# Optimization experiments

Measured on AMD Instinct MI355X. Metric: run time of the kernel, lower is better.

The kernel has to match this reference:

```python
import jax, jax.numpy as jnp
import numpy as np

S, DM, H, DH, FF, L = 2048, 1024, 16, 64, 4096, 2
N_IMG, GH, GW = 4, 16, 32  # 4 images, each 16x32=512 tokens
THETA = 10000.0
LN_EPS = 1e-5


def _rope_tables():
    # 2D repeated rope: dim=DH, dim//4 freqs, x/y angles interleaved -> DH//2 per token
    fr = 1.0 / THETA ** (np.arange(0, DH, 4)[: DH // 4] / DH)  # [DH//4]
    pos = np.arange(GH * GW)
    xang = np.outer(pos % GW, fr)   # [512, DH//4]
    yang = np.outer(pos // GW, fr)  # [512, DH//4]
    ang = np.stack([xang, yang], axis=-1).reshape(GH * GW, DH // 2)  # [512, DH//2]
    ang = np.tile(ang, (N_IMG, 1))  # same grid repeated per image -> [S, DH//2]
    return np.cos(ang).astype(np.float32), np.sin(ang).astype(np.float32)


def setup_inputs() -> dict:
    key = jax.random.key(0)
    ks = jax.random.split(key, 8)
    scale = 0.02

    def rn(k, shape):
        return jax.random.normal(k, shape, jnp.float32) * scale

    x = jax.random.normal(ks[0], (S, DM), jnp.float32)
    input_row_offsets = jnp.array([0, 512, 1024, 1536, 2048], jnp.int32)
    cos_np, sin_np = _rope_tables()
    inp = {
        "x": x,
        "input_row_offsets": input_row_offsets,
        "freqs_cos": jnp.asarray(cos_np),
        "freqs_sin": jnp.asarray(sin_np),
        # stacked per-layer params [L, ...]; Linear weights stored as [in, out]
        "ln0_g": jnp.ones((L, DM), jnp.float32),
        "ln0_b": jnp.zeros((L, DM), jnp.float32),
        "ln1_g": jnp.ones((L, DM), jnp.float32),
        "ln1_b": jnp.zeros((L, DM), jnp.float32),
        "wqkv_w": rn(ks[1], (L, DM, 3 * DM)),
        "wqkv_b": jnp.zeros((L, 3 * DM), jnp.float32),
        "wo_w": rn(ks[2], (L, DM, DM)),
        "wo_b": jnp.zeros((L, DM), jnp.float32),
        "up_w": rn(ks[3], (L, DM, FF)),
        "up_b": jnp.zeros((L, FF), jnp.float32),
        "down_w": rn(ks[4], (L, FF, DM)),
        "down_b": jnp.zeros((L, DM), jnp.float32),
        "lnf_g": jnp.ones((DM,), jnp.float32),
        "lnf_b": jnp.zeros((DM,), jnp.float32),
    }
    return inp


def _layernorm(v, g, b):
    m = v.mean(-1, keepdims=True)
    var = v.var(-1, keepdims=True)
    return (v - m) * jax.lax.rsqrt(var + LN_EPS) * g + b


def _rope(t, cos, sin):
    # t: [S, H, DH]; pairs (even, odd) rotated by complex freqs (broadcast over heads)
    tr = t.reshape(S, H, DH // 2, 2)
    te, to = tr[..., 0], tr[..., 1]
    c = cos[:, None, :]
    s = sin[:, None, :]
    oe = te * c - to * s
    oo = te * s + to * c
    return jnp.stack([oe, oo], axis=-1).reshape(S, H, DH)


def reference(x, input_row_offsets, freqs_cos, freqs_sin,
              ln0_g, ln0_b, ln1_g, ln1_b, wqkv_w, wqkv_b, wo_w, wo_b,
              up_w, up_b, down_w, down_b, lnf_g, lnf_b):
    # Block-diagonal mask. NOTE: the torch reference ADDS the boolean mask
    # (True -> +1.0) to the logits, it does NOT mask with -inf. Replicated faithfully.
    seg = jnp.searchsorted(input_row_offsets, jnp.arange(S), side="right")
    maskf = (seg[:, None] == seg[None, :]).astype(jnp.float32)  # [S, S]
    inv_sqrt_d = 1.0 / jnp.sqrt(jnp.float32(DH))

    def layer(h, p):
        g0, b0, g1, b1, Wqkv, bqkv, Wo, bo, Wu, bu, Wd, bd = p
        y = _layernorm(h, g0, b0)
        qkv = (y @ Wqkv + bqkv).reshape(S, 3, H, DH)
        q, k, v = qkv[:, 0], qkv[:, 1], qkv[:, 2]
        q = _rope(q, freqs_cos, freqs_sin)
        k = _rope(k, freqs_cos, freqs_sin)
        aw = jnp.einsum("shd,thd->hst", q, k) * inv_sqrt_d + maskf[None]  # [H,S,S]
        aw = jax.nn.softmax(aw.astype(jnp.float32), axis=-1).astype(q.dtype)
        ao = jnp.einsum("hst,thd->shd", aw, v).reshape(S, DM)
        h = h + ao @ Wo + bo
        y = _layernorm(h, g1, b1)
        y = jax.nn.gelu(y @ Wu + bu, approximate=True)
        h = h + y @ Wd + bd
        return h, None

    params = (ln0_g, ln0_b, ln1_g, ln1_b, wqkv_w, wqkv_b, wo_w, wo_b,
              up_w, up_b, down_w, down_b)
    h, _ = jax.lax.scan(layer, x, params)
    return _layernorm(h, lnf_g, lnf_b)
```

## Files before the change

### kernel.cpp

```cpp
#include <hip/hip_runtime.h>
#include <hip/hip_bf16.h>
#include <stdint.h>
#include <math.h>

#define S_LEN 2048
#define DMODEL 1024
#define NHEAD 16
#define DHEAD 64
#define FFDIM 4096
#define NLAYER 2

using bf16 = __hip_bfloat16;
typedef __attribute__((ext_vector_type(8))) short bf16x8;
typedef __attribute__((ext_vector_type(4))) float f32x4;
typedef __attribute__((ext_vector_type(16))) float f32x16;
typedef __attribute__((ext_vector_type(4))) int i32x4;

#define MFMA16x16(A, B, C) __builtin_amdgcn_mfma_f32_16x16x32_bf16(A, B, C, 0, 0, 0)
#define MFMA32x32(A, B, C) __builtin_amdgcn_mfma_f32_32x32x16_bf16(A, B, C, 0, 0, 0)
#define EXP2(x) __builtin_amdgcn_exp2f(x)

__device__ __forceinline__ float bf2f(uint32_t u16bits) {
  union { uint32_t i; float f; } x;
  x.i = u16bits << 16;
  return x.f;
}
__device__ __forceinline__ uint16_t f2bf(float f) {
  return __builtin_bit_cast(uint16_t, __float2bfloat16(f));
}

__device__ __forceinline__ uint32_t cvtpk(float lo, float hi) {
  uint32_t r;
  asm("v_cvt_pk_bf16_f32 %0, %1, %2" : "=v"(r) : "v"(lo), "v"(hi));
  return r;
}
__device__ __forceinline__ void pl32swap(uint32_t& a, uint32_t& b) {
#if __has_builtin(__builtin_amdgcn_permlane32_swap)
  typedef __attribute__((ext_vector_type(2))) int i32x2;
  i32x2 r = __builtin_amdgcn_permlane32_swap((int)a, (int)b, false, false);
  a = (uint32_t)r.x;
  b = (uint32_t)r.y;
#else
  asm volatile("v_permlane32_swap_b32 %0, %1" : "+v"(a), "+v"(b));
#endif
}

__global__ __launch_bounds__(256) void k_tcast(const float* __restrict__ in,
                                               bf16* __restrict__ out,
                                               int R, int C) {
  __shared__ float tl[32][33];
  int t = threadIdx.x;
  int r0 = blockIdx.y * 32, c0 = blockIdx.x * 32;
  int cl = t & 31, rl = t >> 5;
#pragma unroll
  for (int i = 0; i < 4; ++i)
    tl[rl + i * 8][cl] = in[(size_t)(r0 + rl + i * 8) * C + c0 + cl];
  __syncthreads();
#pragma unroll
  for (int i = 0; i < 4; ++i)
    out[(size_t)(c0 + rl + i * 8) * R + r0 + cl] = __float2bfloat16(tl[cl][rl + i * 8]);
}

__device__ __forceinline__ void ln_store4(bf16* p, float a, float b, float c, float d) {
  uint2 u;
  u.x = (uint32_t)f2bf(a) | ((uint32_t)f2bf(b) << 16);
  u.y = (uint32_t)f2bf(c) | ((uint32_t)f2bf(d) << 16);
  *(uint2*)p = u;
}
__device__ __forceinline__ void ln_store4(float* p, float a, float b, float c, float d) {
  *(float4*)p = make_float4(a, b, c, d);
}

template <typename OUT>
__global__ __launch_bounds__(256) void k_ln(const float* __restrict__ h,
                                            const float* __restrict__ g,
                                            const float* __restrict__ b,
                                            OUT* __restrict__ y) {
  int row = blockIdx.x, t = threadIdx.x;
  const float4 v = ((const float4*)(h + (size_t)row * DMODEL))[t];
  float s = v.x + v.y + v.z + v.w;
  float s2 = v.x * v.x + v.y * v.y + v.z * v.z + v.w * v.w;
#pragma unroll
  for (int off = 32; off > 0; off >>= 1) {
    s += __shfl_down(s, off);
    s2 += __shfl_down(s2, off);
  }
  __shared__ float red[8];
  int w = t >> 6;
  if ((t & 63) == 0) { red[w] = s; red[4 + w] = s2; }
  __syncthreads();
  s = red[0] + red[1] + red[2] + red[3];
  s2 = red[4] + red[5] + red[6] + red[7];
  float mean = s * (1.0f / DMODEL);
  float var = s2 * (1.0f / DMODEL) - mean * mean;
  float rstd = rsqrtf(var + 1e-5f);
  float4 gv = ((const float4*)g)[t];
  float4 bv = ((const float4*)b)[t];
  float o0 = (v.x - mean) * rstd * gv.x + bv.x;
  float o1 = (v.y - mean) * rstd * gv.y + bv.y;
  float o2 = (v.z - mean) * rstd * gv.z + bv.z;
  float o3 = (v.w - mean) * rstd * gv.w + bv.w;
  ln_store4(y + (size_t)row * DMODEL + t * 4, o0, o1, o2, o3);
}

__global__ __launch_bounds__(256) void k_rope(const bf16* __restrict__ qkv,
                                              const float* __restrict__ fcos,
                                              const float* __restrict__ fsin,
                                              bf16* __restrict__ qr,
                                              bf16* __restrict__ kr) {
  int idx = blockIdx.x * 256 + threadIdx.x;
  int p = idx & 31;
  int hh = (idx >> 5) & (NHEAD - 1);
  int s = idx >> 9;
  float c = fcos[s * 32 + p], sn = fsin[s * 32 + p];
  int colq = hh * DHEAD + 2 * p;
  uint32_t rq = *(const uint32_t*)(qkv + (size_t)s * 3 * DMODEL + colq);
  uint32_t rk = *(const uint32_t*)(qkv + (size_t)s * 3 * DMODEL + DMODEL + colq);
  {
    float te = bf2f(rq & 0xffffu), to = bf2f(rq >> 16);
    uint32_t outv = (uint32_t)f2bf(te * c - to * sn) | ((uint32_t)f2bf(te * sn + to * c) << 16);
    *(uint32_t*)(qr + (size_t)s * DMODEL + colq) = outv;
  }
  {
    float te = bf2f(rk & 0xffffu), to = bf2f(rk >> 16);
    uint32_t outv = (uint32_t)f2bf(te * c - to * sn) | ((uint32_t)f2bf(te * sn + to * c) << 16);
    *(uint32_t*)(kr + (size_t)s * DMODEL + colq) = outv;
  }
}

__global__ __launch_bounds__(256) void k_tv(const bf16* __restrict__ qkv,
                                            bf16* __restrict__ vT) {
  __shared__ bf16 tl[64][65];
  int t = threadIdx.x;
  int hh = blockIdx.y;
  int sb = blockIdx.x * 64;
#pragma unroll
  for (int i = 0; i < 16; ++i) {
    int e = i * 256 + t;
    int sl = e >> 6, d = e & 63;
    tl[sl][d] = qkv[(size_t)(sb + sl) * 3 * DMODEL + 2 * DMODEL + hh * DHEAD + d];
  }
  __syncthreads();
#pragma unroll
  for (int i = 0; i < 16; ++i) {
    int e = i * 256 + t;
    int d = e >> 6, sl = e & 63;
    vT[(size_t)(hh * DHEAD + d) * S_LEN + sb + sl] = tl[sl][d];
  }
}

template <int EPI, int BM>
__global__ __launch_bounds__(256) void k_gemm2(const bf16* __restrict__ A,
                                               const bf16* __restrict__ BT,
                                               const float* __restrict__ bias,
                                               void* __restrict__ out,
                                               int M, int N, int K, int Kc) {
  constexpr int MF = BM / 32;
  __shared__ bf16 As[2][BM * 64];
  __shared__ bf16 Bs[2][128 * 64];
  int t = threadIdx.x;
  int w = t >> 6, l = t & 63, lr = l & 15, lg = l >> 4;

  int nxy = gridDim.x * gridDim.y;
  int bid = blockIdx.y * gridDim.x + blockIdx.x;
  int chk8 = nxy >> 3;
  int swz = (bid & 7) * chk8 + (bid >> 3);
  int bx = swz % gridDim.x, by = swz / gridDim.x;
  int bm = bx * BM, bn = by * 128;
  int k0 = blockIdx.z * Kc;
  int wm = (w >> 1) * (BM / 2), wn = (w & 1) * 64;

  f32x4 zero4 = {0.f, 0.f, 0.f, 0.f};
  f32x4 acc[MF][4];
#pragma unroll
  for (int mf = 0; mf < MF; ++mf)
#pragma unroll
    for (int nf = 0; nf < 4; ++nf) acc[mf][nf] = zero4;

  auto stage = [&](int buf, int kk) {
#pragma unroll
    for (int i = 0; i < BM / 32; ++i) {
      int chunk = i * 256 + t;
      int row = chunk >> 3;
      int scol = ((chunk ^ row) & 7) << 3;
      __builtin_amdgcn_global_load_lds(
          (__attribute__((address_space(1))) void*)(A + (size_t)(bm + row) * K + kk + scol),
          (__attribute__((address_space(3))) void*)(&As[buf][chunk * 8]), 16, 0, 0);
    }
#pragma unroll
    for (int i = 0; i < 4; ++i) {
      int chunk = i * 256 + t;
      int row = chunk >> 3;
      int scol = ((chunk ^ row) & 7) << 3;
      __builtin_amdgcn_global_load_lds(
          (__attribute__((address_space(1))) void*)(BT + (size_t)(bn + row) * K + kk + scol),
          (__attribute__((address_space(3))) void*)(&Bs[buf][chunk * 8]), 16, 0, 0);
    }
  };

  int nt = Kc / 64;
  stage(0, k0);
  __syncthreads();
  int cur = 0;
  for (int kt = 0; kt < nt; ++kt) {
    bf16x8 af[2][MF], bfr[2][4];
#pragma unroll
    for (int h = 0; h < 2; ++h) {
#pragma unroll
      for (int mf = 0; mf < MF; ++mf) {
        int row = wm + mf * 16 + lr;
        af[h][mf] = *(const bf16x8*)(&As[cur][row * 64 + ((((h << 2) + lg) ^ (row & 7)) << 3)]);
      }
#pragma unroll
      for (int nf = 0; nf < 4; ++nf) {
        int row = wn + nf * 16 + lr;
        bfr[h][nf] = *(const bf16x8*)(&Bs[cur][row * 64 + ((((h << 2) + lg) ^ (row & 7)) << 3)]);
      }
    }
    __builtin_amdgcn_sched_barrier(0);
    if (kt + 1 < nt) stage(cur ^ 1, k0 + (kt + 1) * 64);
    __builtin_amdgcn_sched_barrier(0);
#pragma unroll
    for (int h = 0; h < 2; ++h)
#pragma unroll
      for (int mf = 0; mf < MF; ++mf)
#pragma unroll
        for (int nf = 0; nf < 4; ++nf)
          acc[mf][nf] = MFMA16x16(af[h][mf], bfr[h][nf], acc[mf][nf]);
    __syncthreads();
    cur ^= 1;
  }

  if (EPI == 3) {
    float* outf = (float*)out + (size_t)blockIdx.z * ((size_t)M * N);
#pragma unroll
    for (int mf = 0; mf < MF; ++mf)
#pragma unroll
      for (int nf = 0; nf < 4; ++nf) {
        int col = bn + wn + nf * 16 + lr;
        int row0 = bm + wm + mf * 16 + lg * 4;
#pragma unroll
        for (int r = 0; r < 4; ++r)
          outf[(size_t)(row0 + r) * N + col] = acc[mf][nf][r];
      }
  } else {
    bf16* outb = (bf16*)out;
#pragma unroll
    for (int mf = 0; mf < MF; ++mf)
#pragma unroll
      for (int nf = 0; nf < 4; ++nf) {
        int col = bn + wn + nf * 16 + lr;
        float bv = bias[col];
        int row0 = bm + wm + mf * 16 + lg * 4;
#pragma unroll
        for (int r = 0; r < 4; ++r) {
          float v = acc[mf][nf][r] + bv;
          if (EPI == 2)
            v = 0.5f * v * (1.0f + tanhf(0.7978845608028654f * (v + 0.044715f * v * v * v)));
          outb[(size_t)(row0 + r) * N + col] = __float2bfloat16(v);
        }
      }
  }
}

template <int KS>
__global__ __launch_bounds__(256) void k_reduce(const float* __restrict__ part,
                                                const float* __restrict__ bias,
                                                float* __restrict__ hb,
                                                int MN, int N) {
  int i4 = (blockIdx.x * 256 + threadIdx.x) * 4;
  float4 r = *(const float4*)(hb + i4);
  float4 b = *(const float4*)(bias + (i4 & (N - 1)));
  float sx = r.x + b.x, sy = r.y + b.y, sz = r.z + b.z, sw = r.w + b.w;
#pragma unroll
  for (int ks = 0; ks < KS; ++ks) {
    float4 p = *(const float4*)(part + (size_t)ks * MN + i4);
    sx += p.x; sy += p.y; sz += p.z; sw += p.w;
  }
  *(float4*)(hb + i4) = make_float4(sx, sy, sz, sw);
}

__global__ __launch_bounds__(256, 4) void k_attn(const bf16* __restrict__ qr,
                                                 const bf16* __restrict__ kr,
                                                 const bf16* __restrict__ vT,
                                                 const int* __restrict__ offs,
                                                 bf16* __restrict__ ao) {
  __shared__ float oO[4][64][33];
  __shared__ float mM[4][32];
  __shared__ float lL[4][32];

  int t = threadIdx.x, w = t >> 6, l = t & 63;
  int ql = l & 31, hi = l >> 5, hi8 = hi * 8;
  int hh = blockIdx.x, qb = blockIdx.y * 32;
  int h64 = hh * DHEAD;

  constexpr float LOG2E = 1.4426950408889634f;
  constexpr float C1 = 0.125f * LOG2E;

  int q = qb + ql;
  int o0 = offs[0], o1 = offs[1], o2 = offs[2], o3 = offs[3], o4 = offs[4];
  int sl0 = -1073741824, sh0 = 1073741824;
  sl0 = (o0 <= q) ? o0 : sl0;
  sl0 = (o1 <= q) ? o1 : sl0;
  sl0 = (o2 <= q) ? o2 : sl0;
  sl0 = (o3 <= q) ? o3 : sl0;
  sl0 = (o4 <= q) ? o4 : sl0;
  sh0 = (o4 > q) ? o4 : sh0;
  sh0 = (o3 > q) ? o3 : sh0;
  sh0 = (o2 > q) ? o2 : sh0;
  sh0 = (o1 > q) ? o1 : sh0;
  sh0 = (o0 > q) ? o0 : sh0;
  uint32_t spanu = (uint32_t)(sh0 - sl0);

  const bf16* qbase = qr + (size_t)q * DMODEL + h64 + hi8;
  bf16x8 qf0 = *(const bf16x8*)(qbase);
  bf16x8 qf1 = *(const bf16x8*)(qbase + 16);
  bf16x8 qf2 = *(const bf16x8*)(qbase + 32);
  bf16x8 qf3 = *(const bf16x8*)(qbase + 48);

  f32x16 oC0, oC1;
#pragma unroll
  for (int r = 0; r < 16; ++r) { oC0[r] = 0.f; oC1[r] = 0.f; }
  float m_r = -1e30f, l_r = 0.f;

  const bf16* vrow = vT + (size_t)(h64 + ql) * S_LEN + hi8;

  for (int it = 0; it < 16; ++it) {
    int j0 = w * 512 + it * 32;
    const bf16* kbase = kr + (size_t)(j0 + ql) * DMODEL + h64 + hi8;
    bf16x8 kf0 = *(const bf16x8*)(kbase);
    bf16x8 kf1 = *(const bf16x8*)(kbase + 16);
    bf16x8 kf2 = *(const bf16x8*)(kbase + 32);
    bf16x8 kf3 = *(const bf16x8*)(kbase + 48);
    f32x16 sC;
#pragma unroll
    for (int r = 0; r < 16; ++r) sC[r] = 0.f;
    __builtin_amdgcn_s_setprio(1);
    sC = MFMA32x32(kf0, qf0, sC);
    sC = MFMA32x32(kf1, qf1, sC);
    sC = MFMA32x32(kf2, qf2, sC);
    sC = MFMA32x32(kf3, qf3, sC);
    __builtin_amdgcn_s_setprio(0);

    int tt = j0 + hi * 4 - sl0;
#pragma unroll
    for (int r = 0; r < 16; ++r) {
      int ku = tt + ((r & 3) + 8 * (r >> 2));
      float bias = ((uint32_t)ku < spanu) ? LOG2E : 0.0f;
      sC[r] = sC[r] * C1 + bias;
    }
    float rm = sC[0];
#pragma unroll
    for (int r = 1; r < 16; ++r) rm = fmaxf(rm, sC[r]);
    uint32_t ra = __builtin_bit_cast(uint32_t, rm), rb = ra;
    pl32swap(ra, rb);
    float rmax = fmaxf(__builtin_bit_cast(float, ra), __builtin_bit_cast(float, rb));

    if (__any(rmax > m_r + 8.0f)) {
      float mn = fmaxf(m_r, rmax);
      float fs = EXP2(m_r - mn);
      m_r = mn;
      l_r *= fs;
#pragma unroll
      for (int r = 0; r < 16; ++r) { oC0[r] *= fs; oC1[r] *= fs; }
    }
#pragma unroll
    for (int r = 0; r < 16; ++r) {
      float pv = EXP2(sC[r] - m_r);
      sC[r] = pv;
      l_r += pv;
    }
    uint32_t u0 = cvtpk(sC[0], sC[1]), u1 = cvtpk(sC[2], sC[3]);
    uint32_t u2 = cvtpk(sC[4], sC[5]), u3 = cvtpk(sC[6], sC[7]);
    uint32_t u4 = cvtpk(sC[8], sC[9]), u5 = cvtpk(sC[10], sC[11]);
    uint32_t u6 = cvtpk(sC[12], sC[13]), u7 = cvtpk(sC[14], sC[15]);
    pl32swap(u0, u2);
    pl32swap(u1, u3);
    pl32swap(u4, u6);
    pl32swap(u5, u7);
    i32x4 pi0 = {(int)u0, (int)u1, (int)u2, (int)u3};
    i32x4 pi1 = {(int)u4, (int)u5, (int)u6, (int)u7};
    bf16x8 pb0 = __builtin_bit_cast(bf16x8, pi0);
    bf16x8 pb1 = __builtin_bit_cast(bf16x8, pi1);

    const bf16* vbase = vrow + j0;
    bf16x8 va00 = *(const bf16x8*)(vbase);
    bf16x8 va01 = *(const bf16x8*)(vbase + 16);
    bf16x8 va10 = *(const bf16x8*)(vbase + 32 * S_LEN);
    bf16x8 va11 = *(const bf16x8*)(vbase + 32 * S_LEN + 16);
    __builtin_amdgcn_s_setprio(1);
    oC0 = MFMA32x32(va00, pb0, oC0);
    oC0 = MFMA32x32(va01, pb1, oC0);
    oC1 = MFMA32x32(va10, pb0, oC1);
    oC1 = MFMA32x32(va11, pb1, oC1);
    __builtin_amdgcn_s_setprio(0);
  }

  {
    uint32_t la = __builtin_bit_cast(uint32_t, l_r), lb = la;
    pl32swap(la, lb);
    l_r = __builtin_bit_cast(float, la) + __builtin_bit_cast(float, lb);
  }
  if (hi == 0) {
    mM[w][ql] = m_r;
    lL[w][ql] = l_r;
  }
#pragma unroll
  for (int r = 0; r < 16; ++r) {
    int d = (r & 3) + 8 * (r >> 2) + 4 * hi;
    oO[w][d][ql] = oC0[r];
    oO[w][d + 32][ql] = oC1[r];
  }
  __syncthreads();

  {
    int mq = t & 31, dbse = (t >> 5) * 8;
    float m0 = mM[0][mq], m1 = mM[1][mq], m2 = mM[2][mq], m3 = mM[3][mq];
    float ms = fmaxf(fmaxf(m0, m1), fmaxf(m2, m3));
    float a0 = EXP2(m0 - ms), a1 = EXP2(m1 - ms), a2 = EXP2(m2 - ms), a3 = EXP2(m3 - ms);
    float ll = a0 * lL[0][mq] + a1 * lL[1][mq] + a2 * lL[2][mq] + a3 * lL[3][mq];
    float inv = 1.0f / ll;
    uint4 pkv;
    uint32_t pw[4];
#pragma unroll
    for (int i = 0; i < 4; ++i) {
      int d0 = dbse + 2 * i, d1 = dbse + 2 * i + 1;
      float e0 = (a0 * oO[0][d0][mq] + a1 * oO[1][d0][mq] + a2 * oO[2][d0][mq] +
                  a3 * oO[3][d0][mq]) * inv;
      float e1 = (a0 * oO[0][d1][mq] + a1 * oO[1][d1][mq] + a2 * oO[2][d1][mq] +
                  a3 * oO[3][d1][mq]) * inv;
      pw[i] = (uint32_t)f2bf(e0) | ((uint32_t)f2bf(e1) << 16);
    }
    pkv.x = pw[0]; pkv.y = pw[1]; pkv.z = pw[2]; pkv.w = pw[3];
    *(uint4*)(ao + (size_t)(qb + mq) * DMODEL + h64 + dbse) = pkv;
  }
}

extern "C" void kernel_launch(void* const* d_in, const int* in_sizes, int n_in,
                              void* d_out, int out_size, void* d_ws, size_t ws_size,
                              hipStream_t stream) {
  const float* x = (const float*)d_in[0];
  const int* offs = (const int*)d_in[1];
  const float* fcos = (const float*)d_in[2];
  const float* fsin = (const float*)d_in[3];
  const float* ln0g = (const float*)d_in[4];
  const float* ln0b = (const float*)d_in[5];
  const float* ln1g = (const float*)d_in[6];
  const float* ln1b = (const float*)d_in[7];
  const float* wqkv = (const float*)d_in[8];
  const float* bqkv = (const float*)d_in[9];
  const float* wo = (const float*)d_in[10];
  const float* bo = (const float*)d_in[11];
  const float* wu = (const float*)d_in[12];
  const float* bu = (const float*)d_in[13];
  const float* wd = (const float*)d_in[14];
  const float* bd = (const float*)d_in[15];
  const float* lnfg = (const float*)d_in[16];
  const float* lnfb = (const float*)d_in[17];

  char* ws = (char*)d_ws;
  size_t off = 0;
  auto alloc = [&](size_t bytes) -> void* {
    void* p = ws + off;
    off += (bytes + 255) & ~(size_t)255;
    return p;
  };
  bf16* wqkvT = (bf16*)alloc((size_t)NLAYER * 3 * DMODEL * DMODEL * 2);
  bf16* woT = (bf16*)alloc((size_t)NLAYER * DMODEL * DMODEL * 2);
  bf16* wuT = (bf16*)alloc((size_t)NLAYER * DMODEL * FFDIM * 2);
  bf16* wdT = (bf16*)alloc((size_t)NLAYER * FFDIM * DMODEL * 2);
  float* hbuf = (float*)alloc((size_t)S_LEN * DMODEL * 4);
  bf16* ybuf = (bf16*)alloc((size_t)S_LEN * DMODEL * 2);
  bf16* qkv = (bf16*)alloc((size_t)S_LEN * 3 * DMODEL * 2);
  bf16* qrb = (bf16*)alloc((size_t)S_LEN * DMODEL * 2);
  bf16* krb = (bf16*)alloc((size_t)S_LEN * DMODEL * 2);
  bf16* vTb = (bf16*)alloc((size_t)S_LEN * DMODEL * 2);
  bf16* aob = (bf16*)alloc((size_t)S_LEN * DMODEL * 2);
  bf16* midb = (bf16*)alloc((size_t)S_LEN * FFDIM * 2);

  float* partWO = (float*)qkv;
  float* partDN = (float*)ybuf;

  for (int ly = 0; ly < NLAYER; ++ly) {
    k_tcast<<<dim3(3 * DMODEL / 32, DMODEL / 32), 256, 0, stream>>>(
        wqkv + (size_t)ly * DMODEL * 3 * DMODEL, wqkvT + (size_t)ly * 3 * DMODEL * DMODEL, DMODEL, 3 * DMODEL);
    k_tcast<<<dim3(DMODEL / 32, DMODEL / 32), 256, 0, stream>>>(
        wo + (size_t)ly * DMODEL * DMODEL, woT + (size_t)ly * DMODEL * DMODEL, DMODEL, DMODEL);
    k_tcast<<<dim3(FFDIM / 32, DMODEL / 32), 256, 0, stream>>>(
        wu + (size_t)ly * DMODEL * FFDIM, wuT + (size_t)ly * DMODEL * FFDIM, DMODEL, FFDIM);
    k_tcast<<<dim3(DMODEL / 32, FFDIM / 32), 256, 0, stream>>>(
        wd + (size_t)ly * FFDIM * DMODEL, wdT + (size_t)ly * FFDIM * DMODEL, FFDIM, DMODEL);
  }
  hipMemcpyAsync(hbuf, x, (size_t)S_LEN * DMODEL * 4, hipMemcpyDeviceToDevice, stream);

  for (int ly = 0; ly < NLAYER; ++ly) {
    k_ln<bf16><<<S_LEN, 256, 0, stream>>>(hbuf, ln0g + ly * DMODEL, ln0b + ly * DMODEL, ybuf);
    k_gemm2<0, 128><<<dim3(S_LEN / 128, 3 * DMODEL / 128, 1), 256, 0, stream>>>(
        ybuf, wqkvT + (size_t)ly * 3 * DMODEL * DMODEL, bqkv + ly * 3 * DMODEL, qkv,
        S_LEN, 3 * DMODEL, DMODEL, DMODEL);
    k_rope<<<S_LEN * NHEAD * 32 / 256, 256, 0, stream>>>(qkv, fcos, fsin, qrb, krb);
    k_tv<<<dim3(S_LEN / 64, NHEAD), 256, 0, stream>>>(qkv, vTb);
    k_attn<<<dim3(NHEAD, S_LEN / 32), 256, 0, stream>>>(qrb, krb, vTb, offs, aob);
    k_gemm2<3, 64><<<dim3(S_LEN / 64, DMODEL / 128, 2), 256, 0, stream>>>(
        aob, woT + (size_t)ly * DMODEL * DMODEL, nullptr, partWO,
        S_LEN, DMODEL, DMODEL, DMODEL / 2);
    k_reduce<2><<<S_LEN * DMODEL / 1024, 256, 0, stream>>>(
        partWO, bo + ly * DMODEL, hbuf, S_LEN * DMODEL, DMODEL);
    k_ln<bf16><<<S_LEN, 256, 0, stream>>>(hbuf, ln1g + ly * DMODEL, ln1b + ly * DMODEL, ybuf);
    k_gemm2<2, 128><<<dim3(S_LEN / 128, FFDIM / 128, 1), 256, 0, stream>>>(
        ybuf, wuT + (size_t)ly * DMODEL * FFDIM, bu + ly * FFDIM, midb,
        S_LEN, FFDIM, DMODEL, DMODEL);
    k_gemm2<3, 128><<<dim3(S_LEN / 128, DMODEL / 128, 4), 256, 0, stream>>>(
        midb, wdT + (size_t)ly * FFDIM * DMODEL, nullptr, partDN,
        S_LEN, DMODEL, FFDIM, FFDIM / 4);
    k_reduce<4><<<S_LEN * DMODEL / 1024, 256, 0, stream>>>(
        partDN, bd + ly * DMODEL, hbuf, S_LEN * DMODEL, DMODEL);
  }
  k_ln<float><<<S_LEN, 256, 0, stream>>>(hbuf, lnfg, lnfb, (float*)d_out);
}
```

Measured before the change: 407.0 us.

## Split attention key range across eight waves per block with bf16 LDS merge

The attention kernel now uses 512 threads (8 waves) per 32-query block, so each wave processes 256 keys instead of 512 and the loop runs 8 iterations instead of 16. The cross-wave partial outputs are staged in LDS as bf16 instead of fp32 to keep shared memory small, and the final merge combines eight partial softmax states. This aims to shorten the serial key loop per wave and raise occupancy. In exchange the merge does more work, and the partial outputs lose precision when rounded to bf16.

```diff
diff --git a/kernel.cpp b/kernel.cpp
--- a/kernel.cpp
+++ b/kernel.cpp
@@ -280,14 +280,14 @@
   *(float4*)(hb + i4) = make_float4(sx, sy, sz, sw);
 }
 
-__global__ __launch_bounds__(256, 4) void k_attn(const bf16* __restrict__ qr,
+__global__ __launch_bounds__(512, 6) void k_attn(const bf16* __restrict__ qr,
                                                  const bf16* __restrict__ kr,
                                                  const bf16* __restrict__ vT,
                                                  const int* __restrict__ offs,
                                                  bf16* __restrict__ ao) {
-  __shared__ float oO[4][64][33];
-  __shared__ float mM[4][32];
-  __shared__ float lL[4][32];
+  __shared__ bf16 oOb[8][64][36];
+  __shared__ float mM[8][32];
+  __shared__ float lL[8][32];
 
   int t = threadIdx.x, w = t >> 6, l = t & 63;
   int ql = l & 31, hi = l >> 5, hi8 = hi * 8;
@@ -325,8 +325,8 @@
 
   const bf16* vrow = vT + (size_t)(h64 + ql) * S_LEN + hi8;
 
-  for (int it = 0; it < 16; ++it) {
-    int j0 = w * 512 + it * 32;
+  for (int it = 0; it < 8; ++it) {
+    int j0 = w * 256 + it * 32;
     const bf16* kbase = kr + (size_t)(j0 + ql) * DMODEL + h64 + hi8;
     bf16x8 kf0 = *(const bf16x8*)(kbase);
     bf16x8 kf1 = *(const bf16x8*)(kbase + 16);
@@ -408,31 +408,40 @@
 #pragma unroll
   for (int r = 0; r < 16; ++r) {
     int d = (r & 3) + 8 * (r >> 2) + 4 * hi;
-    oO[w][d][ql] = oC0[r];
-    oO[w][d + 32][ql] = oC1[r];
+    oOb[w][d][ql] = __float2bfloat16(oC0[r]);
+    oOb[w][d + 32][ql] = __float2bfloat16(oC1[r]);
   }
   __syncthreads();
 
   {
-    int mq = t & 31, dbse = (t >> 5) * 8;
-    float m0 = mM[0][mq], m1 = mM[1][mq], m2 = mM[2][mq], m3 = mM[3][mq];
-    float ms = fmaxf(fmaxf(m0, m1), fmaxf(m2, m3));
-    float a0 = EXP2(m0 - ms), a1 = EXP2(m1 - ms), a2 = EXP2(m2 - ms), a3 = EXP2(m3 - ms);
-    float ll = a0 * lL[0][mq] + a1 * lL[1][mq] + a2 * lL[2][mq] + a3 * lL[3][mq];
+    int mq = t & 31, dbse = (t >> 5) * 4;
+    float mv0 = mM[0][mq], mv1 = mM[1][mq], mv2 = mM[2][mq], mv3 = mM[3][mq];
+    float mv4 = mM[4][mq], mv5 = mM[5][mq], mv6 = mM[6][mq], mv7 = mM[7][mq];
+    float ms = fmaxf(fmaxf(fmaxf(mv0, mv1), fmaxf(mv2, mv3)),
+                     fmaxf(fmaxf(mv4, mv5), fmaxf(mv6, mv7)));
+    float a0 = EXP2(mv0 - ms), a1 = EXP2(mv1 - ms), a2 = EXP2(mv2 - ms), a3 = EXP2(mv3 - ms);
+    float a4 = EXP2(mv4 - ms), a5 = EXP2(mv5 - ms), a6 = EXP2(mv6 - ms), a7 = EXP2(mv7 - ms);
+    float ll = a0 * lL[0][mq] + a1 * lL[1][mq] + a2 * lL[2][mq] + a3 * lL[3][mq] +
+               a4 * lL[4][mq] + a5 * lL[5][mq] + a6 * lL[6][mq] + a7 * lL[7][mq];
     float inv = 1.0f / ll;
-    uint4 pkv;
-    uint32_t pw[4];
-#pragma unroll
-    for (int i = 0; i < 4; ++i) {
+    uint32_t pw[2];
+#pragma unroll
+    for (int i = 0; i < 2; ++i) {
       int d0 = dbse + 2 * i, d1 = dbse + 2 * i + 1;
-      float e0 = (a0 * oO[0][d0][mq] + a1 * oO[1][d0][mq] + a2 * oO[2][d0][mq] +
-                  a3 * oO[3][d0][mq]) * inv;
-      float e1 = (a0 * oO[0][d1][mq] + a1 * oO[1][d1][mq] + a2 * oO[2][d1][mq] +
-                  a3 * oO[3][d1][mq]) * inv;
-      pw[i] = (uint32_t)f2bf(e0) | ((uint32_t)f2bf(e1) << 16);
-    }
-    pkv.x = pw[0]; pkv.y = pw[1]; pkv.z = pw[2]; pkv.w = pw[3];
-    *(uint4*)(ao + (size_t)(qb + mq) * DMODEL + h64 + dbse) = pkv;
+      float e0 = a0 * __bfloat162float(oOb[0][d0][mq]) + a1 * __bfloat162float(oOb[1][d0][mq]) +
+                 a2 * __bfloat162float(oOb[2][d0][mq]) + a3 * __bfloat162float(oOb[3][d0][mq]) +
+                 a4 * __bfloat162float(oOb[4][d0][mq]) + a5 * __bfloat162float(oOb[5][d0][mq]) +
+                 a6 * __bfloat162float(oOb[6][d0][mq]) + a7 * __bfloat162float(oOb[7][d0][mq]);
+      float e1 = a0 * __bfloat162float(oOb[0][d1][mq]) + a1 * __bfloat162float(oOb[1][d1][mq]) +
+                 a2 * __bfloat162float(oOb[2][d1][mq]) + a3 * __bfloat162float(oOb[3][d1][mq]) +
+                 a4 * __bfloat162float(oOb[4][d1][mq]) + a5 * __bfloat162float(oOb[5][d1][mq]) +
+                 a6 * __bfloat162float(oOb[6][d1][mq]) + a7 * __bfloat162float(oOb[7][d1][mq]);
+      pw[i] = (uint32_t)f2bf(e0 * inv) | ((uint32_t)f2bf(e1 * inv) << 16);
+    }
+    uint2 pkv;
+    pkv.x = pw[0];
+    pkv.y = pw[1];
+    *(uint2*)(ao + (size_t)(qb + mq) * DMODEL + h64 + dbse) = pkv;
   }
 }
 
@@ -500,7 +509,7 @@
         S_LEN, 3 * DMODEL, DMODEL, DMODEL);
     k_rope<<<S_LEN * NHEAD * 32 / 256, 256, 0, stream>>>(qkv, fcos, fsin, qrb, krb);
     k_tv<<<dim3(S_LEN / 64, NHEAD), 256, 0, stream>>>(qkv, vTb);
-    k_attn<<<dim3(NHEAD, S_LEN / 32), 256, 0, stream>>>(qrb, krb, vTb, offs, aob);
+    k_attn<<<dim3(NHEAD, S_LEN / 32), 512, 0, stream>>>(qrb, krb, vTb, offs, aob);
     k_gemm2<3, 64><<<dim3(S_LEN / 64, DMODEL / 128, 2), 256, 0, stream>>>(
         aob, woT + (size_t)ly * DMODEL * DMODEL, nullptr, partWO,
         S_LEN, DMODEL, DMODEL, DMODEL / 2);
```

Result: slower. 454.1 us (+11.6%).
